# Kernel optimization log

Measured on AMD Instinct MI355X. Metric: run time of the kernel, lower is better.

## Reference

```python
import jax, jax.numpy as jnp
import numpy as np

N, E, G, F, H, L = 50000, 400000, 64, 7, 300, 100


def setup_inputs() -> dict:
    key = jax.random.key(0)
    ks = jax.random.split(key, 24)
    w = lambda k, i, o: jax.random.normal(k, (i, o), jnp.float32) * 0.05
    return {
        "x": jax.random.normal(ks[0], (N, F), jnp.float32),
        "edge_index": jax.random.randint(ks[1], (2, E), 0, N),
        "batch": jnp.sort(jax.random.randint(ks[2], (N,), 0, G)),
        "u": jax.random.normal(ks[3], (G, 2), jnp.float32),
        # EdgeLayer 0: mlp(2*F -> H -> H -> L)
        "l0_w1": w(ks[4], 2 * F, H), "l0_b1": jnp.zeros((H,), jnp.float32),
        "l0_w2": w(ks[5], H, H),     "l0_b2": jnp.zeros((H,), jnp.float32),
        "l0_w3": w(ks[6], H, L),     "l0_b3": jnp.zeros((L,), jnp.float32),
        # EdgeLayer 1: mlp(2*L -> H -> H -> L)
        "l1_w1": w(ks[7], 2 * L, H), "l1_b1": jnp.zeros((H,), jnp.float32),
        "l1_w2": w(ks[8], H, H),     "l1_b2": jnp.zeros((H,), jnp.float32),
        "l1_w3": w(ks[9], H, L),     "l1_b3": jnp.zeros((L,), jnp.float32),
        # final lin: (3*L + 2) -> L -> L -> 2
        "lin_w1": w(ks[10], 3 * L + 2, L), "lin_b1": jnp.zeros((L,), jnp.float32),
        "lin_w2": w(ks[11], L, L),          "lin_b2": jnp.zeros((L,), jnp.float32),
        "lin_w3": w(ks[12], L, 2),          "lin_b3": jnp.zeros((2,), jnp.float32),
    }


def mlp3(h, w1, b1, w2, b2, w3, b3):
    h = jax.nn.relu(h @ w1 + b1)
    h = jax.nn.relu(h @ w2 + b2)
    return h @ w3 + b3


def edge_layer(x, src, dst, w1, b1, w2, b2, w3, b3):
    # gather endpoints, per-edge MLP on [x_i, x_j - x_i], scatter-max to target nodes
    xi = x[dst]          # [E, C] target (x_i)
    xj = x[src]          # [E, C] source (x_j)
    msg = mlp3(jnp.concatenate([xi, xj - xi], axis=-1), w1, b1, w2, b2, w3, b3)
    n = x.shape[0]
    agg = jax.ops.segment_max(msg, dst, num_segments=n)
    cnt = jax.ops.segment_sum(jnp.ones((msg.shape[0], 1), msg.dtype), dst, num_segments=n)
    return jnp.where(cnt > 0, agg, 0.0)  # PyG fills empty neighborhoods with 0


def reference(x, edge_index, batch, u,
              l0_w1, l0_b1, l0_w2, l0_b2, l0_w3, l0_b3,
              l1_w1, l1_b1, l1_w2, l1_b2, l1_w3, l1_b3,
              lin_w1, lin_b1, lin_w2, lin_b2, lin_w3, lin_b3):
    src, dst = edge_index[0], edge_index[1]
    h = jax.nn.relu(edge_layer(x, src, dst, l0_w1, l0_b1, l0_w2, l0_b2, l0_w3, l0_b3))
    h = jax.nn.relu(edge_layer(h, src, dst, l1_w1, l1_b1, l1_w2, l1_b2, l1_w3, l1_b3))
    # global add / mean / max pooling per graph
    addp = jax.ops.segment_sum(h, batch, num_segments=G)
    cnt = jax.ops.segment_sum(jnp.ones((h.shape[0], 1), h.dtype), batch, num_segments=G)
    meanp = addp / jnp.maximum(cnt, 1.0)
    maxp = jax.ops.segment_max(h, batch, num_segments=G)
    maxp = jnp.where(cnt > 0, maxp, 0.0)
    pooled = jnp.concatenate([addp, meanp, maxp, u], axis=1)  # [G, 3L+2]
    return mlp3(pooled, lin_w1, lin_b1, lin_w2, lin_b2, lin_w3, lin_b3)
```

## Files before the change

kernel.cpp:

```cpp
#include <hip/hip_runtime.h>

typedef unsigned short u16;
typedef short s16x8 __attribute__((ext_vector_type(8)));
typedef float f32x4 __attribute__((ext_vector_type(4)));

#define DI __device__ __forceinline__

constexpr int N_ = 50000;
constexpr int E_ = 400000;
constexpr int G_ = 64;
constexpr int MS_ = 112;
constexpr int UVS_ = 608;

DI u16 f2bf(float f) {
    union { unsigned u; float f; } c; c.f = f;
    unsigned u = c.u;
    u += 0x7fffu + ((u >> 16) & 1u);
    return (u16)(u >> 16);
}
DI float bf2f(u16 v) {
    union { unsigned u; float f; } c; c.u = (unsigned)v << 16;
    return c.f;
}
DI unsigned pkbf(float lo, float hi) {
    return (unsigned)f2bf(lo) | ((unsigned)f2bf(hi) << 16);
}

DI s16x8 ldv(const u16* p) { return *(const s16x8*)p; }
DI f32x4 MFMA(s16x8 a, s16x8 b, f32x4 c) {
    return __builtin_amdgcn_mfma_f32_16x16x32_bf16(a, b, c, 0, 0, 0);
}

DI s16x8 conv_frag(const f32x4 a0, const f32x4 a1, int kq, int col) {
    unsigned c0 = pkbf(fmaxf(a0[0], 0.f), fmaxf(a0[1], 0.f));
    unsigned c1 = pkbf(fmaxf(a0[2], 0.f), fmaxf(a0[3], 0.f));
    unsigned c2 = pkbf(fmaxf(a1[0], 0.f), fmaxf(a1[1], 0.f));
    unsigned c3 = pkbf(fmaxf(a1[2], 0.f), fmaxf(a1[3], 0.f));
    int aA = (kq & 1) * 128 + col * 4;
    int aB = aA + 64;
    unsigned A0 = __builtin_amdgcn_ds_bpermute(aA, (int)c0);
    unsigned A1 = __builtin_amdgcn_ds_bpermute(aA, (int)c1);
    unsigned A2 = __builtin_amdgcn_ds_bpermute(aA, (int)c2);
    unsigned A3 = __builtin_amdgcn_ds_bpermute(aA, (int)c3);
    unsigned B0 = __builtin_amdgcn_ds_bpermute(aB, (int)c0);
    unsigned B1 = __builtin_amdgcn_ds_bpermute(aB, (int)c1);
    unsigned B2 = __builtin_amdgcn_ds_bpermute(aB, (int)c2);
    unsigned B3 = __builtin_amdgcn_ds_bpermute(aB, (int)c3);
    bool hi = (kq >> 1) != 0;
    union { unsigned u[4]; s16x8 v; } o;
    o.u[0] = hi ? A2 : A0;
    o.u[1] = hi ? A3 : A1;
    o.u[2] = hi ? B2 : B0;
    o.u[3] = hi ? B3 : B1;
    return o.v;
}

__global__ __launch_bounds__(256)
void ModelGNN_35304631174019_kernel(
          const float* __restrict__ l0w1, const float* __restrict__ l0w2,
          const float* __restrict__ l0w3, const float* __restrict__ l1w1,
          const float* __restrict__ l1w2, const float* __restrict__ l1w3,
          const float* __restrict__ l0b1, const float* __restrict__ l0b2,
          const float* __restrict__ l0b3, const float* __restrict__ l1b1,
          const float* __restrict__ l1b2, const float* __restrict__ l1b3,
          float4* __restrict__ histz,
          u16* __restrict__ wtu0, u16* __restrict__ wtu1,
          u16* __restrict__ wt2a, u16* __restrict__ wt2b,
          u16* __restrict__ wt3a, u16* __restrict__ wt3b)
{
    int i = blockIdx.x * 256 + threadIdx.x;
    if (i < 12500) { histz[i] = make_float4(0.f, 0.f, 0.f, 0.f); return; }
    int f = i - 12500;

    if (f < 19456) {
        int sec = f >> 9, w = f & 511;
        int col = w >> 5, kq = (w & 31) >> 3, j = w & 7;
        int chunk = sec >> 1, b01 = sec & 1;
        int n = chunk * 32 + b01 * 16 + col;
        int k = kq * 8 + j;
        u16 v = 0;
        if (k < 7) {
            if (n < 300)                  v = f2bf(l0w1[k * 300 + n] - l0w1[(7 + k) * 300 + n]);
            else if (n >= 304 && n < 604) v = f2bf(l0w1[(7 + k) * 300 + (n - 304)]);
        } else if (k == 7) {
            if (n < 300) v = f2bf(l0b1[n]);
        }
        wtu0[f] = v; return;
    }
    f -= 19456;
    if (f < 77824) {
        int sec = f >> 9, w = f & 511;
        int col = w >> 5, kq = (w & 31) >> 3, j = w & 7;
        int chunk = sec >> 3, r = sec & 7, s = r >> 1, b01 = r & 1;
        int n = chunk * 32 + b01 * 16 + col;
        int k = s * 32 + kq * 8 + j;
        u16 v = 0;
        if (k < 100) {
            if (n < 300)                  v = f2bf(l1w1[k * 300 + n] - l1w1[(100 + k) * 300 + n]);
            else if (n >= 304 && n < 604) v = f2bf(l1w1[(100 + k) * 300 + (n - 304)]);
        } else if (k == 100) {
            if (n < 300) v = f2bf(l1b1[n]);
        }
        wtu1[f] = v; return;
    }
    f -= 77824;
    if (f < 204800) {
        const float* src = (f < 102400) ? l0w2 : l1w2;
        const float* bia = (f < 102400) ? l0b2 : l1b2;
        u16* dst = (f < 102400) ? wt2a : wt2b;
        int f2 = (f < 102400) ? f : f - 102400;
        int sec = f2 >> 9, w = f2 & 511;
        int col = w >> 5, rem = w & 31;
        int n0c = sec / 20, r = sec % 20;
        int s = r >> 1, b01 = r & 1;
        int n = n0c * 32 + b01 * 16 + col, k = s * 32 + rem;
        u16 v = 0;
        if (n < 300) {
            if (k < 300)       v = f2bf(src[k * 300 + n]);
            else if (k == 300) v = f2bf(bia[n]);
        }
        dst[f2] = v;
        return;
    }
    f -= 204800;
    if (f < 71680) {
        const float* src = (f < 35840) ? l0w3 : l1w3;
        const float* bia = (f < 35840) ? l0b3 : l1b3;
        u16* dst = (f < 35840) ? wt3a : wt3b;
        int f2 = (f < 35840) ? f : f - 35840;
        int sec = f2 >> 9, w = f2 & 511;
        int col = w >> 5, rem = w & 31;
        int ch = sec / 7, u = sec % 7;
        int n3 = u * 16 + col, k = ch * 32 + rem;
        u16 v = 0;
        if (n3 < 100) {
            if (k < 300)       v = f2bf(src[k * 100 + n3]);
            else if (k == 300) v = f2bf(bia[n3]);
        }
        dst[f2] = v;
        return;
    }
}

__global__ __launch_bounds__(256)
void hist_k(const int* __restrict__ ei, int* __restrict__ hist)
{
    int i = blockIdx.x * 256 + threadIdx.x;
    if (i < E_) atomicAdd(&hist[ei[E_ + i]], 1);
}

__global__ __launch_bounds__(1024)
void scan_k(int* h)
{
    __shared__ int part[1024];
    const int t = threadIdx.x;
    const int CH = 49;
    int base = t * CH;
    int end = base + CH; if (end > 50000) end = 50000;
    int s = 0;
    for (int i = base; i < end; ++i) s += h[i];
    part[t] = s;
    __syncthreads();
    for (int d = 1; d < 1024; d <<= 1) {
        int v = (t >= d) ? part[t - d] : 0;
        __syncthreads();
        part[t] += v;
        __syncthreads();
    }
    int run = (t ? part[t - 1] : 0);
    for (int i = base; i < end; ++i) { int c = h[i]; h[i] = run; run += c; }
}

__global__ __launch_bounds__(256)
void fill_k(const int* __restrict__ ei, int* __restrict__ pos, int* __restrict__ sei)
{
    int i = blockIdx.x * 256 + threadIdx.x;
    if (i >= E_) return;
    int s = ei[i], d = ei[E_ + i];
    int p = atomicAdd(&pos[d], 1);
    sei[p] = s; sei[E_ + p] = d;
}

template<int KA>
__global__ __launch_bounds__(256, 2)
void gemm_uv(const float* __restrict__ A, const u16* __restrict__ W,
             float* __restrict__ UV)
{
    __shared__ __align__(16) float SC[4][1024];
    const int tid = threadIdx.x, wave = tid >> 6, lane = tid & 63;
    const int col = lane & 15, kq = lane >> 4;
    const int nb = blockIdx.x * 128 + wave * 32;
    const int fragoff = col * 32 + kq * 8;

    s16x8 aF[2][KA];
    #pragma unroll
    for (int rt = 0; rt < 2; ++rt) {
        int node = nb + rt * 16 + col; if (node >= N_) node = N_ - 1;
        if constexpr (KA == 1) {
            s16x8 t = {0, 0, 0, 0, 0, 0, 0, 0};
            if (kq == 0) {
                const float* r = A + (size_t)node * 7;
                #pragma unroll
                for (int j = 0; j < 7; ++j) t[j] = (short)f2bf(r[j]);
                t[7] = (short)0x3f80;
            }
            aF[rt][0] = t;
        } else {
            const float* r = A + (size_t)node * 100;
            #pragma unroll
            for (int s = 0; s < KA; ++s) {
                int k0 = s * 32 + kq * 8;
                s16x8 t = {0, 0, 0, 0, 0, 0, 0, 0};
                if (k0 + 8 <= 100) {
                    float4 a = *(const float4*)(r + k0);
                    float4 b = *(const float4*)(r + k0 + 4);
                    t[0] = (short)f2bf(a.x); t[1] = (short)f2bf(a.y);
                    t[2] = (short)f2bf(a.z); t[3] = (short)f2bf(a.w);
                    t[4] = (short)f2bf(b.x); t[5] = (short)f2bf(b.y);
                    t[6] = (short)f2bf(b.z); t[7] = (short)f2bf(b.w);
                } else if (k0 == 96) {
                    float4 a = *(const float4*)(r + 96);
                    t[0] = (short)f2bf(a.x); t[1] = (short)f2bf(a.y);
                    t[2] = (short)f2bf(a.z); t[3] = (short)f2bf(a.w);
                    t[4] = (short)0x3f80;
                }
                aF[rt][s] = t;
            }
        }
    }

    float* SCw = SC[wave];
    #pragma unroll 1
    for (int c = 0; c < 19; ++c) {
        const u16* w0 = W + (size_t)(c * 2 * KA) * 512 + fragoff;
        s16x8 wb[2 * KA];
        #pragma unroll
        for (int t = 0; t < 2 * KA; ++t) wb[t] = ldv(w0 + t * 512);
        f32x4 z = {0.f, 0.f, 0.f, 0.f};
        f32x4 ac[2][2] = {{z, z}, {z, z}};
        #pragma unroll
        for (int s = 0; s < KA; ++s)
            #pragma unroll
            for (int rt = 0; rt < 2; ++rt) {
                ac[0][rt] = MFMA(wb[2 * s],     aF[rt][s], ac[0][rt]);
                ac[1][rt] = MFMA(wb[2 * s + 1], aF[rt][s], ac[1][rt]);
            }
        #pragma unroll
        for (int cb = 0; cb < 2; ++cb)
            #pragma unroll
            for (int rt = 0; rt < 2; ++rt)
                #pragma unroll
                for (int r = 0; r < 4; ++r)
                    SCw[(rt * 16 + col) * 32 + cb * 16 + kq * 4 + r] = ac[cb][rt][r];
        #pragma unroll
        for (int p = 0; p < 4; ++p) {
            int row = p * 8 + (lane >> 3);
            int node = nb + row;
            if (node < N_) {
                float4 v = *(const float4*)(SCw + row * 32 + (lane & 7) * 4);
                *(float4*)(UV + (size_t)node * UVS_ + c * 32 + (lane & 7) * 4) = v;
            }
        }
    }
}

#define COMPUTE2(W2R, W3R, CH) {                                              \
    f32x4 z_ = {0.f, 0.f, 0.f, 0.f};                                          \
    f32x4 ac_[2][2] = {{z_, z_}, {z_, z_}};                                   \
    _Pragma("unroll")                                                         \
    for (int s_ = 0; s_ < 10; ++s_) {                                         \
        _Pragma("unroll")                                                     \
        for (int rt_ = 0; rt_ < 2; ++rt_) {                                   \
            ac_[0][rt_] = MFMA(W2R[2 * s_],     a2[rt_][s_], ac_[0][rt_]);    \
            ac_[1][rt_] = MFMA(W2R[2 * s_ + 1], a2[rt_][s_], ac_[1][rt_]);    \
        }                                                                     \
    }                                                                         \
    s16x8 a3_[2];                                                             \
    _Pragma("unroll")                                                         \
    for (int rt_ = 0; rt_ < 2; ++rt_)                                         \
        a3_[rt_] = conv_frag(ac_[0][rt_], ac_[1][rt_], kq, col);              \
    if ((CH) == 9 && kq == 1) {                                               \
        a3_[0][4] = (short)0x3f80;                                            \
        a3_[1][4] = (short)0x3f80;                                            \
    }                                                                         \
    _Pragma("unroll")                                                         \
    for (int u_ = 0; u_ < 7; ++u_) {                                          \
        mac[0][u_] = MFMA(W3R[u_], a3_[0], mac[0][u_]);                       \
        mac[1][u_] = MFMA(W3R[u_], a3_[1], mac[1][u_]);                       \
    }                                                                         \
}

__global__ __launch_bounds__(256, 1)
void edge_uv(const float* __restrict__ UV, const int* __restrict__ ei,
             const u16* __restrict__ W2, const u16* __restrict__ W3,
             u16* __restrict__ msg)
{
    __shared__ __align__(16) u16 SCR[4 * 32 * MS_];

    const int tid  = threadIdx.x;
    const int wave = tid >> 6, lane = tid & 63;
    const int col  = lane & 15, kq = lane >> 4;
    const int ebase = blockIdx.x * 128 + wave * 32;
    const int fragoff = col * 32 + kq * 8;

    u16* SCw = SCR + wave * (32 * MS_);

    s16x8 a2[2][10];
    #pragma unroll
    for (int rt = 0; rt < 2; ++rt) {
        const int e = ebase + rt * 16 + col;
        const int dn = ei[E_ + e];
        const int sn = ei[e];
        const float* Ud = UV + (size_t)dn * UVS_;
        const float* Vs = UV + (size_t)sn * UVS_ + 304;
        #pragma unroll
        for (int h = 0; h < 2; ++h) {
            float4 ua[5], ub[5], va[5], vb[5];
            #pragma unroll
            for (int q = 0; q < 5; ++q) {
                int k0 = (h * 5 + q) * 32 + kq * 8;
                const float4 zz = make_float4(0.f, 0.f, 0.f, 0.f);
                bool ok = (k0 <= 296);
                ua[q] = ok ? *(const float4*)(Ud + k0)     : zz;
                ub[q] = ok ? *(const float4*)(Ud + k0 + 4) : zz;
                va[q] = ok ? *(const float4*)(Vs + k0)     : zz;
                vb[q] = ok ? *(const float4*)(Vs + k0 + 4) : zz;
            }
            #pragma unroll
            for (int q = 0; q < 5; ++q) {
                unsigned p0 = pkbf(fmaxf(ua[q].x + va[q].x, 0.f),
                                   fmaxf(ua[q].y + va[q].y, 0.f));
                unsigned p1 = pkbf(fmaxf(ua[q].z + va[q].z, 0.f),
                                   fmaxf(ua[q].w + va[q].w, 0.f));
                unsigned p2 = pkbf(fmaxf(ub[q].x + vb[q].x, 0.f),
                                   fmaxf(ub[q].y + vb[q].y, 0.f));
                unsigned p3 = pkbf(fmaxf(ub[q].z + vb[q].z, 0.f),
                                   fmaxf(ub[q].w + vb[q].w, 0.f));
                union { unsigned u[4]; s16x8 v; } o;
                o.u[0] = p0; o.u[1] = p1; o.u[2] = p2; o.u[3] = p3;
                a2[rt][h * 5 + q] = o.v;
            }
        }
    }
    if (kq == 1) {
        a2[0][9][4] = (short)0x3f80;
        a2[1][9][4] = (short)0x3f80;
    }

    f32x4 mac[2][7];
    #pragma unroll
    for (int rt = 0; rt < 2; ++rt)
        #pragma unroll
        for (int u = 0; u < 7; ++u) { f32x4 z = {0.f, 0.f, 0.f, 0.f}; mac[rt][u] = z; }

    {
        s16x8 w2A[20], w3A[7], w2B[20], w3B[7];
        #pragma unroll
        for (int s = 0; s < 20; ++s) w2A[s] = ldv(W2 + s * 512 + fragoff);
        #pragma unroll
        for (int u = 0; u < 7; ++u)  w3A[u] = ldv(W3 + u * 512 + fragoff);
        #pragma unroll 1
        for (int ch = 0; ch < 10; ch += 2) {
            #pragma unroll
            for (int s = 0; s < 20; ++s)
                w2B[s] = ldv(W2 + (size_t)(ch + 1) * 20 * 512 + s * 512 + fragoff);
            #pragma unroll
            for (int u = 0; u < 7; ++u)
                w3B[u] = ldv(W3 + (size_t)(ch + 1) * 7 * 512 + u * 512 + fragoff);
            COMPUTE2(w2A, w3A, ch);
            if (ch + 2 < 10) {
                #pragma unroll
                for (int s = 0; s < 20; ++s)
                    w2A[s] = ldv(W2 + (size_t)(ch + 2) * 20 * 512 + s * 512 + fragoff);
                #pragma unroll
                for (int u = 0; u < 7; ++u)
                    w3A[u] = ldv(W3 + (size_t)(ch + 2) * 7 * 512 + u * 512 + fragoff);
            }
            COMPUTE2(w2B, w3B, ch + 1);
        }
    }

    #pragma unroll
    for (int rt = 0; rt < 2; ++rt) {
        const int row = rt * 16 + col;
        #pragma unroll
        for (int u = 0; u < 7; ++u) {
            unsigned p0 = pkbf(fmaxf(mac[rt][u][0], 0.f), fmaxf(mac[rt][u][1], 0.f));
            unsigned p1 = pkbf(fmaxf(mac[rt][u][2], 0.f), fmaxf(mac[rt][u][3], 0.f));
            int chb = u * 16 + kq * 4;
            *(unsigned*)(SCw + row * MS_ + chb)     = p0;
            *(unsigned*)(SCw + row * MS_ + chb + 2) = p1;
        }
    }
    u16* gdst = msg + (size_t)ebase * MS_;
    #pragma unroll
    for (int q2 = 0; q2 < 7; ++q2) {
        s16x8 v = ldv(SCw + q2 * 512 + lane * 8);
        *(s16x8*)(gdst + q2 * 512 + lane * 8) = v;
    }
}

__global__ __launch_bounds__(256)
void reduce_k(const u16* __restrict__ msg, const int* __restrict__ pos,
              float* __restrict__ agg)
{
    const int n = blockIdx.x * 4 + (threadIdx.x >> 6);
    if (n >= N_) return;
    const int lane = threadIdx.x & 63;
    const int start = n ? pos[n - 1] : 0;
    const int end   = pos[n];
    float m0 = 0.f, m1 = 0.f;
    for (int e = start; e < end; ++e) {
        const u16* row = msg + (size_t)e * MS_;
        m0 = fmaxf(m0, bf2f(row[lane]));
        if (lane < 36) m1 = fmaxf(m1, bf2f(row[64 + lane]));
    }
    agg[(size_t)n * 100 + lane] = m0;
    if (lane < 36) agg[(size_t)n * 100 + 64 + lane] = m1;
}

__global__ __launch_bounds__(256)
void pool(const float* __restrict__ agg1, const int* __restrict__ batch,
          const float* __restrict__ u, float* __restrict__ pooled)
{
    const int g = blockIdx.x;
    int lo = 0, hi = N_;
    while (lo < hi) { int mid = (lo + hi) >> 1; if (batch[mid] < g) lo = mid + 1; else hi = mid; }
    const int start = lo;
    int lo2 = start, hi2 = N_;
    while (lo2 < hi2) { int mid = (lo2 + hi2) >> 1; if (batch[mid] < g + 1) lo2 = mid + 1; else hi2 = mid; }
    const int end = lo2;

    const int c = threadIdx.x & 127, half = threadIdx.x >> 7;
    float sm = 0.f, mx = 0.f;
    if (c < 100)
        for (int n = start + half; n < end; n += 2) {
            float v = agg1[(size_t)n * 100 + c];
            sm += v; mx = fmaxf(mx, v);
        }
    __shared__ float ssum[128], smax[128];
    if (half) { ssum[c] = sm; smax[c] = mx; }
    __syncthreads();
    if (!half && c < 100) {
        sm += ssum[c]; mx = fmaxf(mx, smax[c]);
        int cnt = end - start;
        pooled[g * 302 + c]       = sm;
        pooled[g * 302 + 100 + c] = sm / fmaxf((float)cnt, 1.f);
        pooled[g * 302 + 200 + c] = mx;
    }
    if (threadIdx.x == 0) {
        pooled[g * 302 + 300] = u[g * 2];
        pooled[g * 302 + 301] = u[g * 2 + 1];
    }
}

__global__ __launch_bounds__(128)
void final_mlp(const float* __restrict__ pooled,
               const float* __restrict__ w1, const float* __restrict__ b1,
               const float* __restrict__ w2, const float* __restrict__ b2,
               const float* __restrict__ w3, const float* __restrict__ b3,
               float* __restrict__ out)
{
    const int g = blockIdx.x, t = threadIdx.x;
    __shared__ float P[302], T1[100], T2[100];
    for (int i = t; i < 302; i += 128) P[i] = pooled[g * 302 + i];
    __syncthreads();
    if (t < 100) {
        float a = b1[t];
        for (int i = 0; i < 302; ++i) a = fmaf(P[i], w1[i * 100 + t], a);
        T1[t] = fmaxf(a, 0.f);
    }
    __syncthreads();
    if (t < 100) {
        float a = b2[t];
        for (int i = 0; i < 100; ++i) a = fmaf(T1[i], w2[i * 100 + t], a);
        T2[t] = fmaxf(a, 0.f);
    }
    __syncthreads();
    if (t < 2) {
        float a = b3[t];
        for (int i = 0; i < 100; ++i) a = fmaf(T2[i], w3[i * 2 + t], a);
        out[g * 2 + t] = a;
    }
}

extern "C" void kernel_launch(void* const* d_in, const int* in_sizes, int n_in,
                              void* d_out, int out_size, void* d_ws, size_t ws_size,
                              hipStream_t stream)
{
    const float* x     = (const float*)d_in[0];
    const int*   ei    = (const int*)d_in[1];
    const int*   batch = (const int*)d_in[2];
    const float* uu    = (const float*)d_in[3];
    const float *l0w1 = (const float*)d_in[4],  *l0b1 = (const float*)d_in[5];
    const float *l0w2 = (const float*)d_in[6],  *l0b2 = (const float*)d_in[7];
    const float *l0w3 = (const float*)d_in[8],  *l0b3 = (const float*)d_in[9];
    const float *l1w1 = (const float*)d_in[10], *l1b1 = (const float*)d_in[11];
    const float *l1w2 = (const float*)d_in[12], *l1b2 = (const float*)d_in[13];
    const float *l1w3 = (const float*)d_in[14], *l1b3 = (const float*)d_in[15];
    const float *lw1  = (const float*)d_in[16], *lb1  = (const float*)d_in[17];
    const float *lw2  = (const float*)d_in[18], *lb2  = (const float*)d_in[19];
    const float *lw3  = (const float*)d_in[20], *lb3  = (const float*)d_in[21];

    char* w = (char*)d_ws;
    float* agg0   = (float*)(w);
    float* agg1   = (float*)(w + 20000000);
    float* pooled = (float*)(w + 40000000);
    u16* wtu0 = (u16*)(w + 40077312);
    u16* wtu1 = (u16*)(w + 40116224);
    u16* wt2a = (u16*)(w + 40271872);
    u16* wt2b = (u16*)(w + 40476672);
    u16* wt3a = (u16*)(w + 40681472);
    u16* wt3b = (u16*)(w + 40753152);
    int* hist = (int*)(w + 40824832);
    int* sei  = (int*)(w + 41024832);
    u16* msg  = (u16*)(w + 44224832);
    float* UV = (float*)(w + 133824832);

    ModelGNN_35304631174019_kernel<<<1509, 256, 0, stream>>>(
        l0w1, l0w2, l0w3, l1w1, l1w2, l1w3,
        l0b1, l0b2, l0b3, l1b1, l1b2, l1b3,
        (float4*)hist, wtu0, wtu1, wt2a, wt2b, wt3a, wt3b);
    hist_k<<<1563, 256, 0, stream>>>(ei, hist);
    scan_k<<<1, 1024, 0, stream>>>(hist);
    fill_k<<<1563, 256, 0, stream>>>(ei, hist, sei);
    gemm_uv<1><<<391, 256, 0, stream>>>(x, wtu0, UV);
    edge_uv<<<3125, 256, 0, stream>>>(UV, sei, wt2a, wt3a, msg);
    reduce_k<<<12500, 256, 0, stream>>>(msg, hist, agg0);
    gemm_uv<4><<<391, 256, 0, stream>>>(agg0, wtu1, UV);
    edge_uv<<<3125, 256, 0, stream>>>(UV, sei, wt2b, wt3b, msg);
    reduce_k<<<12500, 256, 0, stream>>>(msg, hist, agg1);
    pool<<<G_, 256, 0, stream>>>(agg1, batch, uu, pooled);
    final_mlp<<<G_, 128, 0, stream>>>(pooled, lw1, lb1, lw2, lb2, lw3, lb3, (float*)d_out);
}
```

Before: 1.179 ms.

## Drop weight double-buffering in edge MLP to allow two blocks per CU

Replaces the double-buffered register prefetch of W2/W3 fragments (two sets of 27 vectors) with a single-buffered per-chunk load. The launch bound changes from one to two blocks per SM so the compiler targets lower register use. The intent is to hide weight-load latency through extra occupancy instead of through software prefetch. The risk is exposed load latency within each wave, and spills if the tighter register budget is not met.

```diff
diff --git a/kernel.cpp b/kernel.cpp
--- a/kernel.cpp
+++ b/kernel.cpp
@@ -290,7 +290,7 @@
     }                                                                         \
 }
 
-__global__ __launch_bounds__(256, 1)
+__global__ __launch_bounds__(256, 2)
 void edge_uv(const float* __restrict__ UV, const int* __restrict__ ei,
              const u16* __restrict__ W2, const u16* __restrict__ W3,
              u16* __restrict__ msg)
@@ -353,30 +353,37 @@
         #pragma unroll
         for (int u = 0; u < 7; ++u) { f32x4 z = {0.f, 0.f, 0.f, 0.f}; mac[rt][u] = z; }
 
-    {
-        s16x8 w2A[20], w3A[7], w2B[20], w3B[7];
-        #pragma unroll
-        for (int s = 0; s < 20; ++s) w2A[s] = ldv(W2 + s * 512 + fragoff);
-        #pragma unroll
-        for (int u = 0; u < 7; ++u)  w3A[u] = ldv(W3 + u * 512 + fragoff);
-        #pragma unroll 1
-        for (int ch = 0; ch < 10; ch += 2) {
+    #pragma unroll 1
+    for (int ch = 0; ch < 10; ++ch) {
+        const u16* w0 = W2 + (size_t)(ch * 20) * 512 + fragoff;
+        s16x8 wb[20];
+        #pragma unroll
+        for (int s = 0; s < 20; ++s) wb[s] = ldv(w0 + s * 512);
+        f32x4 z = {0.f, 0.f, 0.f, 0.f};
+        f32x4 ac[2][2] = {{z, z}, {z, z}};
+        #pragma unroll
+        for (int s = 0; s < 10; ++s)
             #pragma unroll
-            for (int s = 0; s < 20; ++s)
-                w2B[s] = ldv(W2 + (size_t)(ch + 1) * 20 * 512 + s * 512 + fragoff);
-            #pragma unroll
-            for (int u = 0; u < 7; ++u)
-                w3B[u] = ldv(W3 + (size_t)(ch + 1) * 7 * 512 + u * 512 + fragoff);
-            COMPUTE2(w2A, w3A, ch);
-            if (ch + 2 < 10) {
-                #pragma unroll
-                for (int s = 0; s < 20; ++s)
-                    w2A[s] = ldv(W2 + (size_t)(ch + 2) * 20 * 512 + s * 512 + fragoff);
-                #pragma unroll
-                for (int u = 0; u < 7; ++u)
-                    w3A[u] = ldv(W3 + (size_t)(ch + 2) * 7 * 512 + u * 512 + fragoff);
-            }
-            COMPUTE2(w2B, w3B, ch + 1);
+            for (int rt = 0; rt < 2; ++rt) {
+                ac[0][rt] = MFMA(wb[2 * s],     a2[rt][s], ac[0][rt]);
+                ac[1][rt] = MFMA(wb[2 * s + 1], a2[rt][s], ac[1][rt]);
+            }
+        s16x8 w3b[7];
+        #pragma unroll
+        for (int u = 0; u < 7; ++u)
+            w3b[u] = ldv(W3 + (size_t)(ch * 7 + u) * 512 + fragoff);
+        s16x8 a3[2];
+        #pragma unroll
+        for (int rt = 0; rt < 2; ++rt)
+            a3[rt] = conv_frag(ac[0][rt], ac[1][rt], kq, col);
+        if (ch == 9 && kq == 1) {
+            a3[0][4] = (short)0x3f80;
+            a3[1][4] = (short)0x3f80;
+        }
+        #pragma unroll
+        for (int u = 0; u < 7; ++u) {
+            mac[0][u] = MFMA(w3b[u], a3[0], mac[0][u]);
+            mac[1][u] = MFMA(w3b[u], a3[1], mac[1][u]);
         }
     }
 
```

New measurement: 1.221 ms. 1.04x slower.
